# Kernel tuning notes

Hardware: AMD Instinct MI355X
Metric: run time of the kernel (lower is better)

Reference implementation:

```python
import jax, jax.numpy as jnp
import numpy as np

B, T, C, H = 4, 1024, 2048, 16
HD = C // H          # head dim = 128 (even, as RoPE requires)
BLOCK = 1024         # config.block_size == config.max_block_size
NEG = -1e30          # finite stand-in for -inf in the additive attention bias


def setup_inputs() -> dict:
    key = jax.random.key(0)
    k1, k2, k3, k4, k5 = jax.random.split(key, 5)
    x = jax.random.normal(k1, (B, T, C), jnp.float32)
    cumulative_scores = jax.random.uniform(k2, (B, T), jnp.float32)  # kept small: fed to exp()
    token_index = jax.random.randint(k3, (B, T), 0, BLOCK, dtype=jnp.int32)
    padding_mask = jnp.ones((B, T), jnp.int32)
    # xavier-ish scale so softmax doesn't saturate
    W_attn = jax.random.normal(k4, (C, 3 * C), jnp.float32) / np.sqrt(C)
    W_proj = jax.random.normal(k5, (C, C), jnp.float32) / np.sqrt(C)
    return dict(x=x, cumulative_scores=cumulative_scores, token_index=token_index,
                padding_mask=padding_mask, W_attn=W_attn, W_proj=W_proj)


def _rotate_half(a):
    a1, a2 = a[..., : HD // 2], a[..., HD // 2:]
    return jnp.concatenate([-a2, a1], axis=-1)


def reference(x, cumulative_scores, token_index, padding_mask, W_attn, W_proj):
    # QKV projection (bias=False per config)
    qkv = x @ W_attn                                  # (B,T,3C)
    q, k, v = jnp.split(qkv, 3, axis=2)
    heads = lambda a: a.reshape(B, T, H, HD).transpose(0, 2, 1, 3)  # (B,H,T,HD)
    q, k, v = heads(q), heads(k), heads(v)

    # input-dependent partial rotation positions (exact replica of the original
    # scatter: token_index (B,T) fancy-indexes the last axis of a (B,BLOCK)
    # buffer, so counts are summed over ALL batch rows, as in the source)
    counts = jnp.zeros((B, BLOCK), jnp.float32).at[..., token_index].add(1.0)
    t = jnp.cumsum(jnp.take_along_axis(1.0 / (counts + 1e-10), token_index, axis=-1), axis=-1)  # (B,T)

    # RoPE with per-token positions t (seq_dim=-2, offset 0 for both q and k)
    inv_freq = 1.0 / (10000.0 ** (jnp.arange(0, HD, 2, dtype=jnp.float32) / HD))
    freqs = jnp.einsum('bt,j->btj', t, inv_freq)
    emb = jnp.concatenate([freqs, freqs], axis=-1)[:, None, :, :]   # (B,1,T,HD)
    sin, cos = jnp.sin(emb), jnp.cos(emb)
    q = q * cos + _rotate_half(q) * sin
    k = k * cos + _rotate_half(k) * sin

    # 'fork' plan overrides on the last rotary channel
    q = q.at[..., -1].set(1.0)
    k = k.at[..., -1].set(jnp.broadcast_to(cumulative_scores[:, None, :], (B, H, T)))

    # V rescaled by exp(cumulative_scores)
    v = v * jnp.exp(cumulative_scores)[:, None, :, None]

    # causal + key-padding additive bias, SDPA with scale 1/sqrt(HD)
    keep = jnp.tril(jnp.ones((T, T), bool))[None, None] & padding_mask.astype(bool)[:, None, None, :]
    scores = jnp.einsum('bhqd,bhkd->bhqk', q, k) / np.sqrt(HD)
    scores = jnp.where(keep, scores, NEG)
    attn = jax.nn.softmax(scores, axis=-1)
    y = jnp.einsum('bhqk,bhkd->bhqd', attn, v)

    y = y.transpose(0, 2, 1, 3).reshape(B, T, C)
    return y @ W_proj
```

## Files before the change

kernel.cpp:

```cpp
#include <hip/hip_runtime.h>

#define BB 4
#define TT 1024
#define CCH 2048
#define HH 16
#define HDIM 128
#define NBLK 1024
#define MM (BB*TT)
#define N1 (3*CCH)
#define NQT 16

typedef _Float16 f16;
typedef _Float16 half8 __attribute__((ext_vector_type(8)));
typedef _Float16 half4 __attribute__((ext_vector_type(4)));
typedef float floatx4 __attribute__((ext_vector_type(4)));

__device__ __forceinline__ void g2lds16(const void* g, void* l) {
    __builtin_amdgcn_global_load_lds((const __attribute__((address_space(1))) void*)g,
                                     (__attribute__((address_space(3))) void*)l, 16, 0, 0);
}

__global__ void k_prep(const float* __restrict__ Wa, const float* __restrict__ Wp,
                       const float* __restrict__ x,
                       f16* __restrict__ WaT, f16* __restrict__ WpT,
                       f16* __restrict__ x16) {
    int z = blockIdx.z;
    if (z == 2) {
        int i = (blockIdx.y * 192 + blockIdx.x) * 256 + threadIdx.x + threadIdx.y * 32;
        if (i >= MM * CCH / 4) return;
        float4 v = ((const float4*)x)[i];
        union { ushort4 u; f16 h[4]; } o;
        o.h[0] = (f16)v.x; o.h[1] = (f16)v.y; o.h[2] = (f16)v.z; o.h[3] = (f16)v.w;
        ((ushort4*)x16)[i] = o.u;
        return;
    }
    const float* in = (z == 0) ? Wa : Wp;
    f16* out = (z == 0) ? WaT : WpT;
    int Cc = (z == 0) ? N1 : CCH;
    if (blockIdx.x * 32 >= Cc) return;
    __shared__ float tile[32][33];
    int c0 = blockIdx.x * 32, r0 = blockIdx.y * 32;
    int tx = threadIdx.x, ty = threadIdx.y;
#pragma unroll
    for (int k = 0; k < 4; k++) {
        int r = ty + k * 8;
        tile[r][tx] = in[(size_t)(r0 + r) * Cc + c0 + tx];
    }
    __syncthreads();
#pragma unroll
    for (int k = 0; k < 4; k++) {
        int r = ty + k * 8;
        out[(size_t)(c0 + r) * CCH + r0 + tx] = (f16)tile[tx][r];
    }
}

__global__ void k_trv(const f16* __restrict__ in, f16* __restrict__ out) {
    __shared__ f16 tile[32][34];
    int bh = blockIdx.z;
    int h0 = blockIdx.x * 32, t0 = blockIdx.y * 32;
    int tx = threadIdx.x, ty = threadIdx.y;
#pragma unroll
    for (int k = 0; k < 4; k++) {
        int t = ty + k * 8;
        tile[t][tx] = in[((size_t)bh * TT + t0 + t) * HDIM + h0 + tx];
    }
    __syncthreads();
#pragma unroll
    for (int k = 0; k < 4; k++) {
        int r = ty + k * 8;
        out[((size_t)bh * HDIM + h0 + r) * TT + t0 + tx] = tile[tx][r];
    }
}

__global__ void k_hist(const int* __restrict__ tok, int* __restrict__ cnt) {
    int i = blockIdx.x * blockDim.x + threadIdx.x;
    if (i < MM) atomicAdd(cnt + tok[i], 1);
}

__global__ __launch_bounds__(1024) void k_scan(const int* __restrict__ tok,
                                               const int* __restrict__ cnt,
                                               const int* __restrict__ pm,
                                               float* __restrict__ tpos,
                                               float* __restrict__ pb) {
    __shared__ float s[TT];
    int b = blockIdx.x, t = threadIdx.x;
    s[t] = 1.0f / ((float)cnt[tok[b * TT + t]] + 1e-10f);
    __syncthreads();
    for (int off = 1; off < TT; off <<= 1) {
        float add = (t >= off) ? s[t - off] : 0.0f;
        __syncthreads();
        s[t] += add;
        __syncthreads();
    }
    tpos[b * TT + t] = s[t];
    pb[b * TT + t] = pm[b * TT + t] ? 0.0f : -1e30f;
}

template <int MODE>
__global__ __launch_bounds__(256) void k_gemm(const f16* __restrict__ A,
                                              const f16* __restrict__ Bt,
                                              void* __restrict__ Cp,
                                              const float* __restrict__ tpos,
                                              const float* __restrict__ cs,
                                              f16* __restrict__ qr,
                                              f16* __restrict__ kr,
                                              f16* __restrict__ vsc,
                                              int Mdim, int Ndim, int Kdim) {
    const float SCALE = 0.08838834764831845f;
    __shared__ __align__(16) f16 As[128 * 32];
    __shared__ __align__(16) f16 Bs[128 * 32];
    int nbn = Ndim >> 7;
    int bm = blockIdx.x / nbn, bn = blockIdx.x % nbn;
    int tid = threadIdx.x;
    int w = tid >> 6, lane = tid & 63, quad = lane >> 4, l16 = lane & 15;
    int rsub = lane >> 2;
    int csub = (lane & 3) << 3;
    const f16* pa0 = A  + (size_t)((bm << 7) + w * 32 + rsub) * Kdim + csub;
    const f16* pa1 = pa0 + (size_t)16 * Kdim;
    const f16* pb0 = Bt + (size_t)((bn << 7) + w * 32 + rsub) * Kdim + csub;
    const f16* pb1 = pb0 + (size_t)16 * Kdim;
    floatx4 acc[2][8];
#pragma unroll
    for (int i = 0; i < 2; i++)
#pragma unroll
        for (int j = 0; j < 8; j++) acc[i][j] = (floatx4){0.f, 0.f, 0.f, 0.f};
    int nk = Kdim >> 5;
    for (int kt = 0; kt < nk; kt++) {
        __syncthreads();
        g2lds16(pa0, &As[(w * 32) * 32]);
        g2lds16(pa1, &As[(w * 32 + 16) * 32]);
        g2lds16(pb0, &Bs[(w * 32) * 32]);
        g2lds16(pb1, &Bs[(w * 32 + 16) * 32]);
        pa0 += 32; pa1 += 32; pb0 += 32; pb1 += 32;
        __syncthreads();
        half8 af[2], bfr[8];
#pragma unroll
        for (int i = 0; i < 2; i++) af[i] = *(const half8*)&As[(w * 32 + i * 16 + l16) * 32 + (quad << 3)];
#pragma unroll
        for (int j = 0; j < 8; j++) bfr[j] = *(const half8*)&Bs[(j * 16 + l16) * 32 + (quad << 3)];
#pragma unroll
        for (int i = 0; i < 2; i++)
#pragma unroll
            for (int j = 0; j < 8; j++)
                acc[i][j] = __builtin_amdgcn_mfma_f32_16x16x32_f16(af[i], bfr[j], acc[i][j], 0, 0, 0);
    }
    int row0 = (bm << 7) + w * 32 + (quad << 2);
    if (MODE == 0) {
        int cb = (bn << 7) + l16;
#pragma unroll
        for (int i = 0; i < 2; i++)
#pragma unroll
            for (int j = 0; j < 8; j++)
#pragma unroll
                for (int r = 0; r < 4; r++)
                    ((float*)Cp)[(size_t)(row0 + i * 16 + r) * Ndim + cb + j * 16] = acc[i][j][r];
    } else {
        int type = bn >> 4;
        int h = bn & 15;
        if (type < 2) {
            f16* outp = (type == 0) ? qr : kr;
            float invf[4];
#pragma unroll
            for (int jc = 0; jc < 4; jc++)
                invf[jc] = expf((float)(jc * 16 + l16) * -0.14391156929f);
#pragma unroll
            for (int i = 0; i < 2; i++)
#pragma unroll
                for (int r = 0; r < 4; r++) {
                    int row = row0 + i * 16 + r;
                    float tp = tpos[row], csv = cs[row];
                    size_t ob = ((size_t)((row >> 10) * HH + h) * TT + (row & 1023)) * HDIM + l16;
#pragma unroll
                    for (int jc = 0; jc < 4; jc++) {
                        float a1 = acc[i][jc][r], a2 = acc[i][jc + 4][r];
                        float sn, cn;
                        sincosf(tp * invf[jc], &sn, &cn);
                        float o1 = a1 * cn - a2 * sn, o2 = a2 * cn + a1 * sn;
                        if (type == 0) {
                            if (jc == 3 && l16 == 15) o2 = 1.0f;
                            o1 *= SCALE; o2 *= SCALE;
                        } else {
                            if (jc == 3 && l16 == 15) o2 = csv;
                        }
                        outp[ob + jc * 16]      = (f16)o1;
                        outp[ob + jc * 16 + 64] = (f16)o2;
                    }
                }
        } else {
#pragma unroll
            for (int i = 0; i < 2; i++)
#pragma unroll
                for (int r = 0; r < 4; r++) {
                    int row = row0 + i * 16 + r;
                    float ve = expf(cs[row]);
                    size_t ob = ((size_t)((row >> 10) * HH + h) * TT + (row & 1023)) * HDIM + l16;
#pragma unroll
                    for (int jc = 0; jc < 8; jc++)
                        vsc[ob + jc * 16] = (f16)(acc[i][jc][r] * ve);
                }
        }
    }
}

__global__ __launch_bounds__(256) void k_attn(const f16* __restrict__ qr,
                                              const f16* __restrict__ kr,
                                              const f16* __restrict__ vt,
                                              const float* __restrict__ pb,
                                              f16* __restrict__ y) {
    __shared__ __align__(16) f16 Ks[64 * 136];
    __shared__ __align__(16) f16 Vs[128 * 72];
    __shared__ float pbs[64];
    int p = blockIdx.x & (NQT / 2 - 1);
    int bh = blockIdx.x >> 3;
    int b = bh >> 4, h = bh & 15;
    int tid = threadIdx.x;
    int w = tid >> 6, lane = tid & 63, quad = lane >> 4, l16 = lane & 15;
#pragma unroll
    for (int pass = 0; pass < 2; pass++) {
        int qt = pass ? (NQT - 1 - p) : p;
        int q0 = qt << 6;
        int qg = q0 + w * 16 + l16;
        const f16* Qp = qr + ((size_t)bh * TT + qg) * HDIM;
        half8 qf[4];
#pragma unroll
        for (int kc = 0; kc < 4; kc++) qf[kc] = *(const half8*)&Qp[kc * 32 + (quad << 3)];
        floatx4 O[8];
#pragma unroll
        for (int i = 0; i < 8; i++) O[i] = (floatx4){0.f, 0.f, 0.f, 0.f};
        float mx = -1e30f, ls = 0.f;
        for (int kt = 0; kt <= qt; kt++) {
            __syncthreads();
            const f16* Kb = kr + ((size_t)bh * TT + (kt << 6)) * HDIM;
            const f16* Vb = vt + (size_t)bh * HDIM * TT + (kt << 6);
#pragma unroll
            for (int i = 0; i < 4; i++) {
                int seg = tid + (i << 8);
                int krow = seg >> 4, kcol = (seg & 15) << 3;
                *(uint4*)&Ks[krow * 136 + kcol] = *(const uint4*)&Kb[(size_t)krow * HDIM + kcol];
                int vrow = seg >> 3, vcol = (seg & 7) << 3;
                *(uint4*)&Vs[vrow * 72 + vcol] = *(const uint4*)&Vb[(size_t)vrow * TT + vcol];
            }
            if (tid < 64) pbs[tid] = pb[b * TT + (kt << 6) + tid];
            __syncthreads();
            floatx4 Sv[4];
#pragma unroll
            for (int mc = 0; mc < 4; mc++) Sv[mc] = (floatx4){0.f, 0.f, 0.f, 0.f};
#pragma unroll
            for (int kc = 0; kc < 4; kc++)
#pragma unroll
                for (int mc = 0; mc < 4; mc++) {
                    half8 kf = *(const half8*)&Ks[(mc * 16 + l16) * 136 + kc * 32 + (quad << 3)];
                    Sv[mc] = __builtin_amdgcn_mfma_f32_16x16x32_f16(kf, qf[kc], Sv[mc], 0, 0, 0);
                }
            float pv[4][4];
            float mnew = mx;
#pragma unroll
            for (int mc = 0; mc < 4; mc++) {
                float4 pbv = *(const float4*)&pbs[mc * 16 + (quad << 2)];
#pragma unroll
                for (int i = 0; i < 4; i++) {
                    int kv = (kt << 6) + mc * 16 + (quad << 2) + i;
                    float s = (kv <= qg) ? Sv[mc][i] + ((const float*)&pbv)[i] : -1e30f;
                    pv[mc][i] = s;
                    mnew = fmaxf(mnew, s);
                }
            }
            mnew = fmaxf(mnew, __shfl_xor(mnew, 16));
            mnew = fmaxf(mnew, __shfl_xor(mnew, 32));
            float al = __expf(mx - mnew);
            mx = mnew;
            float psum = 0.f;
#pragma unroll
            for (int mc = 0; mc < 4; mc++)
#pragma unroll
                for (int i = 0; i < 4; i++) {
                    float e = __expf(pv[mc][i] - mnew);
                    pv[mc][i] = e;
                    psum += e;
                }
            psum += __shfl_xor(psum, 16);
            psum += __shfl_xor(psum, 32);
            ls = ls * al + psum;
#pragma unroll
            for (int hm = 0; hm < 8; hm++)
#pragma unroll
                for (int i = 0; i < 4; i++) O[hm][i] *= al;
            half4 pf[4];
#pragma unroll
            for (int mc = 0; mc < 4; mc++) {
                pf[mc][0] = (f16)pv[mc][0]; pf[mc][1] = (f16)pv[mc][1];
                pf[mc][2] = (f16)pv[mc][2]; pf[mc][3] = (f16)pv[mc][3];
            }
#pragma unroll
            for (int mc = 0; mc < 4; mc++)
#pragma unroll
                for (int hm = 0; hm < 8; hm++) {
                    half4 vf = *(const half4*)&Vs[(hm * 16 + l16) * 72 + mc * 16 + (quad << 2)];
                    O[hm] = __builtin_amdgcn_mfma_f32_16x16x16f16(vf, pf[mc], O[hm], 0, 0, 0);
                }
        }
        float inv = 1.0f / ls;
#pragma unroll
        for (int hm = 0; hm < 8; hm++) {
            half4 ov;
#pragma unroll
            for (int i = 0; i < 4; i++) ov[i] = (f16)(O[hm][i] * inv);
            *(half4*)&y[((size_t)b * TT + qg) * CCH + h * HDIM + hm * 16 + (quad << 2)] = ov;
        }
        __syncthreads();
    }
}

extern "C" void kernel_launch(void* const* d_in, const int* in_sizes, int n_in,
                              void* d_out, int out_size, void* d_ws, size_t ws_size,
                              hipStream_t stream) {
    const float* x   = (const float*)d_in[0];
    const float* cs  = (const float*)d_in[1];
    const int*   tok = (const int*)d_in[2];
    const int*   pm  = (const int*)d_in[3];
    const float* Wa  = (const float*)d_in[4];
    const float* Wp  = (const float*)d_in[5];
    float* out = (float*)d_out;
    char* ws = (char*)d_ws;

    f16* x16 = (f16*)(ws + 0);
    f16* WaT = (f16*)(ws + 16777216);
    f16* vt  = (f16*)(ws + 41943040);
    f16* WpT = (f16*)(ws + 58720256);
    f16* qr  = (f16*)(ws + 92274688);
    f16* kr  = (f16*)(ws + 109051904);
    f16* vsc = (f16*)(ws + 125829120);
    int*   cnt  = (int*)(ws + 142606336);
    float* tpos = (float*)(ws + 142610432);
    float* pb   = (float*)(ws + 142626816);
    f16* y   = x16;

    hipMemsetAsync(cnt, 0, NBLK * sizeof(int), stream);
    k_hist<<<MM / 256, 256, 0, stream>>>(tok, cnt);
    k_scan<<<BB, TT, 0, stream>>>(tok, cnt, pm, tpos, pb);
    k_prep<<<dim3(N1 / 32, CCH / 32, 3), dim3(32, 8), 0, stream>>>(Wa, Wp, x, WaT, WpT, x16);
    k_gemm<1><<<(MM / 128) * (N1 / 128), 256, 0, stream>>>(x16, WaT, nullptr, tpos, cs,
                                                           qr, kr, vsc, MM, N1, CCH);
    k_trv<<<dim3(4, 32, BB * HH), dim3(32, 8), 0, stream>>>(vsc, vt);
    k_attn<<<BB * HH * (NQT / 2), 256, 0, stream>>>(qr, kr, vt, pb, y);
    k_gemm<0><<<(MM / 128) * (CCH / 128), 256, 0, stream>>>(y, WpT, out, nullptr, nullptr,
                                                            nullptr, nullptr, nullptr, MM, CCH, CCH);
}
```

Measured before the change: 420.3 us.

## Replace GEMM with 256x256 double-buffered, swizzled, 8-wave pipelined kernel and RoPE table

Rewrites both projection GEMMs as a 256x256-tile, 512-thread kernel. It double-buffers LDS through global_load_lds, interleaves staging of the next K tiles with MFMA quarters, and uses an XOR swizzle to avoid LDS bank conflicts. A chiplet-aware block remap groups blocks by XCD. RoPE sin/cos is precomputed into a table by a new small kernel instead of calling sincosf in the GEMM epilogue. The aim is higher MFMA utilisation and less global load latency, at the cost of much more LDS per block (128KB), fewer blocks (384 and 128 on a 256-CU part), and fragile hand-written wait counts.

```diff
diff --git a/kernel.cpp b/kernel.cpp
--- a/kernel.cpp
+++ b/kernel.cpp
@@ -96,107 +96,197 @@
     pb[b * TT + t] = pm[b * TT + t] ? 0.0f : -1e30f;
 }
 
+__global__ void k_rope(const float* __restrict__ tpos, float2* __restrict__ tab) {
+    int i = blockIdx.x * 256 + threadIdx.x;
+    int row = i >> 6, j = i & 63;
+    float f = tpos[row] * expf((float)j * -0.14391156929f);
+    float sn, cn; sincosf(f, &sn, &cn);
+    tab[i] = make_float2(cn, sn);
+}
+
+#define RA(buf, mf, kk) (*(const half8*)((const char*)As + ((buf) << 15) + ((aoffb + ((mf) << 11) + ((kk) << 6)) ^ flip)))
+#define RB(buf, nf, kk) (*(const half8*)((const char*)Bs + ((buf) << 15) + ((boffb + ((nf) << 13) + ((kk) << 6)) ^ flip)))
+#define STAGE(P, L, h, t) do { \
+    g2lds16((P) + (size_t)(((h) << 7) + ro0) * 2048 + ((t) << 6) + co0, (L) + ((h) << 13) + (w << 9)); \
+    g2lds16((P) + (size_t)(((h) << 7) + ro1) * 2048 + ((t) << 6) + co1, (L) + ((h) << 13) + ((8 + w) << 9)); \
+} while (0)
+#define MFMAQ(AF, BF, M0, N0) do { \
+  _Pragma("unroll") for (int m_ = 0; m_ < 4; m_++) \
+  _Pragma("unroll") for (int n_ = 0; n_ < 2; n_++) \
+  _Pragma("unroll") for (int k_ = 0; k_ < 2; k_++) \
+    acc[(M0) + m_][(N0) + n_] = __builtin_amdgcn_mfma_f32_16x16x32_f16(AF[m_][k_], BF[n_][k_], acc[(M0) + m_][(N0) + n_], 0, 0, 0); \
+} while (0)
+#define BAR() __builtin_amdgcn_s_barrier()
+#define WLG0() asm volatile("s_waitcnt lgkmcnt(0)" ::: "memory")
+
 template <int MODE>
-__global__ __launch_bounds__(256) void k_gemm(const f16* __restrict__ A,
-                                              const f16* __restrict__ Bt,
-                                              void* __restrict__ Cp,
-                                              const float* __restrict__ tpos,
-                                              const float* __restrict__ cs,
-                                              f16* __restrict__ qr,
-                                              f16* __restrict__ kr,
-                                              f16* __restrict__ vsc,
-                                              int Mdim, int Ndim, int Kdim) {
+__global__ __launch_bounds__(512, 2) void k_gemm8(const f16* __restrict__ A,
+                                                  const f16* __restrict__ Bt,
+                                                  float* __restrict__ Cp,
+                                                  const float2* __restrict__ tab,
+                                                  const float* __restrict__ cs,
+                                                  f16* __restrict__ qr,
+                                                  f16* __restrict__ kr,
+                                                  f16* __restrict__ vsc) {
     const float SCALE = 0.08838834764831845f;
-    __shared__ __align__(16) f16 As[128 * 32];
-    __shared__ __align__(16) f16 Bs[128 * 32];
-    int nbn = Ndim >> 7;
-    int bm = blockIdx.x / nbn, bn = blockIdx.x % nbn;
+    const int NBN = MODE ? 24 : 8;
+    const int NWG = MODE ? 384 : 128;
+    const int CPX = NWG >> 3;
+    __shared__ __align__(16) f16 As[2 * 16384];
+    __shared__ __align__(16) f16 Bs[2 * 16384];
+
+    int bid = blockIdx.x;
+    int s = (bid & 7) * CPX + (bid >> 3);
+    int bm = s / NBN, bn = s % NBN;
+
     int tid = threadIdx.x;
     int w = tid >> 6, lane = tid & 63, quad = lane >> 4, l16 = lane & 15;
-    int rsub = lane >> 2;
-    int csub = (lane & 3) << 3;
-    const f16* pa0 = A  + (size_t)((bm << 7) + w * 32 + rsub) * Kdim + csub;
-    const f16* pa1 = pa0 + (size_t)16 * Kdim;
-    const f16* pb0 = Bt + (size_t)((bn << 7) + w * 32 + rsub) * Kdim + csub;
-    const f16* pb1 = pb0 + (size_t)16 * Kdim;
-    floatx4 acc[2][8];
-#pragma unroll
-    for (int i = 0; i < 2; i++)
-#pragma unroll
-        for (int j = 0; j < 8; j++) acc[i][j] = (floatx4){0.f, 0.f, 0.f, 0.f};
-    int nk = Kdim >> 5;
-    for (int kt = 0; kt < nk; kt++) {
-        __syncthreads();
-        g2lds16(pa0, &As[(w * 32) * 32]);
-        g2lds16(pa1, &As[(w * 32 + 16) * 32]);
-        g2lds16(pb0, &Bs[(w * 32) * 32]);
-        g2lds16(pb1, &Bs[(w * 32 + 16) * 32]);
-        pa0 += 32; pa1 += 32; pb0 += 32; pb1 += 32;
-        __syncthreads();
-        half8 af[2], bfr[8];
-#pragma unroll
-        for (int i = 0; i < 2; i++) af[i] = *(const half8*)&As[(w * 32 + i * 16 + l16) * 32 + (quad << 3)];
-#pragma unroll
-        for (int j = 0; j < 8; j++) bfr[j] = *(const half8*)&Bs[(j * 16 + l16) * 32 + (quad << 3)];
-#pragma unroll
-        for (int i = 0; i < 2; i++)
-#pragma unroll
-            for (int j = 0; j < 8; j++)
-                acc[i][j] = __builtin_amdgcn_mfma_f32_16x16x32_f16(af[i], bfr[j], acc[i][j], 0, 0, 0);
-    }
-    int row0 = (bm << 7) + w * 32 + (quad << 2);
+    int wm = w >> 2, wn = w & 3;
+
+    const f16* Ab = A + (size_t)(bm << 8) * 2048;
+    const f16* Bb = Bt + (size_t)(bn << 8) * 2048;
+
+    int db0 = (w << 10) + (lane << 4);
+    int db1 = ((8 + w) << 10) + (lane << 4);
+    int sb0 = db0 ^ (((db0 >> 9) & 1) << 5);
+    int sb1 = db1 ^ (((db1 >> 9) & 1) << 5);
+    int ro0 = sb0 >> 7, co0 = (sb0 & 127) >> 1;
+    int ro1 = sb1 >> 7, co1 = (sb1 & 127) >> 1;
+
+    const int flip = (l16 & 4) << 3;
+    const int aoffb = ((wm * 128 + l16) << 7) + (quad << 4);
+    const int boffb = ((wn * 16 + l16) << 7) + (quad << 4);
+
+    floatx4 acc[8][4];
+#pragma unroll
+    for (int i = 0; i < 8; i++)
+#pragma unroll
+        for (int j = 0; j < 4; j++) acc[i][j] = (floatx4){0.f, 0.f, 0.f, 0.f};
+
+    STAGE(Bb, Bs, 0, 0);
+    STAGE(Ab, As, 0, 0);
+    STAGE(Ab, As, 1, 0);
+    STAGE(Bb, Bs, 1, 0);
+    STAGE(Bb, Bs + 16384, 0, 1);
+    STAGE(Ab, As + 16384, 0, 1);
+    STAGE(Ab, As + 16384, 1, 1);
+    asm volatile("s_waitcnt vmcnt(6)" ::: "memory");
+    BAR();
+
+#pragma unroll 1
+    for (int it = 0; it < 16; ++it) {
+        const int t1 = 2 * it + 1, t2 = 2 * it + 2, t3 = 2 * it + 3;
+        const bool g2 = (t2 < 32), g3 = (t3 < 32);
+        half8 af0[4][2], af1[4][2], bf0[2][2], bf1[2][2];
+#pragma unroll
+        for (int m = 0; m < 4; m++) { af0[m][0] = RA(0, m, 0); af0[m][1] = RA(0, m, 1); }
+#pragma unroll
+        for (int n = 0; n < 2; n++) { bf0[n][0] = RB(0, n, 0); bf0[n][1] = RB(0, n, 1); }
+        STAGE(Bb, Bs + 16384, 1, t1);
+        asm volatile("s_waitcnt lgkmcnt(8)" ::: "memory");
+        BAR(); WLG0();
+        __builtin_amdgcn_s_setprio(1); MFMAQ(af0, bf0, 0, 0); __builtin_amdgcn_s_setprio(0);
+        BAR();
+#pragma unroll
+        for (int m = 0; m < 4; m++) { af1[m][0] = RA(0, 4 + m, 0); af1[m][1] = RA(0, 4 + m, 1); }
+        if (g2) STAGE(Bb, Bs, 0, t2);
+        BAR(); WLG0();
+        __builtin_amdgcn_s_setprio(1); MFMAQ(af1, bf0, 4, 0); __builtin_amdgcn_s_setprio(0);
+        BAR();
+#pragma unroll
+        for (int n = 0; n < 2; n++) { bf1[n][0] = RB(0, 2 + n, 0); bf1[n][1] = RB(0, 2 + n, 1); }
+        if (g2) STAGE(Ab, As, 0, t2);
+        BAR(); WLG0();
+        __builtin_amdgcn_s_setprio(1); MFMAQ(af1, bf1, 4, 2); __builtin_amdgcn_s_setprio(0);
+        BAR();
+        if (g2) STAGE(Ab, As, 1, t2);
+        BAR();
+        __builtin_amdgcn_s_setprio(1); MFMAQ(af0, bf1, 0, 2); __builtin_amdgcn_s_setprio(0);
+        if (it < 15) { asm volatile("s_waitcnt vmcnt(6)" ::: "memory"); }
+        else         { asm volatile("s_waitcnt vmcnt(0)" ::: "memory"); }
+        BAR();
+#pragma unroll
+        for (int m = 0; m < 4; m++) { af0[m][0] = RA(1, m, 0); af0[m][1] = RA(1, m, 1); }
+#pragma unroll
+        for (int n = 0; n < 2; n++) { bf0[n][0] = RB(1, n, 0); bf0[n][1] = RB(1, n, 1); }
+        if (g2) STAGE(Bb, Bs, 1, t2);
+        asm volatile("s_waitcnt lgkmcnt(8)" ::: "memory");
+        BAR(); WLG0();
+        __builtin_amdgcn_s_setprio(1); MFMAQ(af0, bf0, 0, 0); __builtin_amdgcn_s_setprio(0);
+        BAR();
+#pragma unroll
+        for (int m = 0; m < 4; m++) { af1[m][0] = RA(1, 4 + m, 0); af1[m][1] = RA(1, 4 + m, 1); }
+        if (g3) STAGE(Bb, Bs + 16384, 0, t3);
+        BAR(); WLG0();
+        __builtin_amdgcn_s_setprio(1); MFMAQ(af1, bf0, 4, 0); __builtin_amdgcn_s_setprio(0);
+        BAR();
+#pragma unroll
+        for (int n = 0; n < 2; n++) { bf1[n][0] = RB(1, 2 + n, 0); bf1[n][1] = RB(1, 2 + n, 1); }
+        if (g3) STAGE(Ab, As + 16384, 0, t3);
+        BAR(); WLG0();
+        __builtin_amdgcn_s_setprio(1); MFMAQ(af1, bf1, 4, 2); __builtin_amdgcn_s_setprio(0);
+        BAR();
+        if (g3) STAGE(Ab, As + 16384, 1, t3);
+        BAR();
+        __builtin_amdgcn_s_setprio(1); MFMAQ(af0, bf1, 0, 2); __builtin_amdgcn_s_setprio(0);
+        if (it < 15) { asm volatile("s_waitcnt vmcnt(6)" ::: "memory"); }
+        else         { asm volatile("s_waitcnt vmcnt(0)" ::: "memory"); }
+        BAR();
+    }
+
     if (MODE == 0) {
-        int cb = (bn << 7) + l16;
-#pragma unroll
-        for (int i = 0; i < 2; i++)
-#pragma unroll
-            for (int j = 0; j < 8; j++)
-#pragma unroll
-                for (int r = 0; r < 4; r++)
-                    ((float*)Cp)[(size_t)(row0 + i * 16 + r) * Ndim + cb + j * 16] = acc[i][j][r];
+#pragma unroll
+        for (int mf = 0; mf < 8; mf++)
+#pragma unroll
+            for (int nf = 0; nf < 4; nf++) {
+                int col = (bn << 8) + wn * 16 + nf * 64 + l16;
+#pragma unroll
+                for (int r = 0; r < 4; r++) {
+                    int row = (bm << 8) + wm * 128 + mf * 16 + (quad << 2) + r;
+                    Cp[(size_t)row * CCH + col] = acc[mf][nf][r];
+                }
+            }
     } else {
-        int type = bn >> 4;
-        int h = bn & 15;
+        int type = bn >> 3;
+        int h0 = (bn * 2) & 15;
+        int d1 = wn * 16 + l16;
         if (type < 2) {
             f16* outp = (type == 0) ? qr : kr;
-            float invf[4];
-#pragma unroll
-            for (int jc = 0; jc < 4; jc++)
-                invf[jc] = expf((float)(jc * 16 + l16) * -0.14391156929f);
-#pragma unroll
-            for (int i = 0; i < 2; i++)
+#pragma unroll
+            for (int mf = 0; mf < 8; mf++)
 #pragma unroll
                 for (int r = 0; r < 4; r++) {
-                    int row = row0 + i * 16 + r;
-                    float tp = tpos[row], csv = cs[row];
-                    size_t ob = ((size_t)((row >> 10) * HH + h) * TT + (row & 1023)) * HDIM + l16;
-#pragma unroll
-                    for (int jc = 0; jc < 4; jc++) {
-                        float a1 = acc[i][jc][r], a2 = acc[i][jc + 4][r];
-                        float sn, cn;
-                        sincosf(tp * invf[jc], &sn, &cn);
-                        float o1 = a1 * cn - a2 * sn, o2 = a2 * cn + a1 * sn;
+                    int row = (bm << 8) + wm * 128 + mf * 16 + (quad << 2) + r;
+                    float2 tc = tab[row * 64 + d1];
+#pragma unroll
+                    for (int p = 0; p < 2; p++) {
+                        float a1 = acc[mf][2 * p][r], a2 = acc[mf][2 * p + 1][r];
+                        float o1 = a1 * tc.x - a2 * tc.y;
+                        float o2 = a2 * tc.x + a1 * tc.y;
                         if (type == 0) {
-                            if (jc == 3 && l16 == 15) o2 = 1.0f;
+                            if (d1 == 63) o2 = 1.0f;
                             o1 *= SCALE; o2 *= SCALE;
                         } else {
-                            if (jc == 3 && l16 == 15) o2 = csv;
+                            if (d1 == 63) o2 = cs[row];
                         }
-                        outp[ob + jc * 16]      = (f16)o1;
-                        outp[ob + jc * 16 + 64] = (f16)o2;
+                        size_t ob = ((size_t)((row >> 10) * HH + h0 + p) * TT + (row & 1023)) * HDIM + d1;
+                        outp[ob] = (f16)o1;
+                        outp[ob + 64] = (f16)o2;
                     }
                 }
         } else {
 #pragma unroll
-            for (int i = 0; i < 2; i++)
+            for (int mf = 0; mf < 8; mf++)
 #pragma unroll
                 for (int r = 0; r < 4; r++) {
-                    int row = row0 + i * 16 + r;
-                    float ve = expf(cs[row]);
-                    size_t ob = ((size_t)((row >> 10) * HH + h) * TT + (row & 1023)) * HDIM + l16;
-#pragma unroll
-                    for (int jc = 0; jc < 8; jc++)
-                        vsc[ob + jc * 16] = (f16)(acc[i][jc][r] * ve);
+                    int row = (bm << 8) + wm * 128 + mf * 16 + (quad << 2) + r;
+                    float ve = __expf(cs[row]);
+#pragma unroll
+                    for (int nf = 0; nf < 4; nf++) {
+                        int d = ((nf & 1) << 6) + d1;
+                        size_t ob = ((size_t)((row >> 10) * HH + h0 + (nf >> 1)) * TT + (row & 1023)) * HDIM + d;
+                        vsc[ob] = (f16)(acc[mf][nf][r] * ve);
+                    }
                 }
         }
     }
@@ -327,6 +417,7 @@
     f16* WaT = (f16*)(ws + 16777216);
     f16* vt  = (f16*)(ws + 41943040);
     f16* WpT = (f16*)(ws + 58720256);
+    float2* tab = (float2*)(ws + 67108864);
     f16* qr  = (f16*)(ws + 92274688);
     f16* kr  = (f16*)(ws + 109051904);
     f16* vsc = (f16*)(ws + 125829120);
@@ -338,11 +429,10 @@
     hipMemsetAsync(cnt, 0, NBLK * sizeof(int), stream);
     k_hist<<<MM / 256, 256, 0, stream>>>(tok, cnt);
     k_scan<<<BB, TT, 0, stream>>>(tok, cnt, pm, tpos, pb);
+    k_rope<<<MM * 64 / 256, 256, 0, stream>>>(tpos, tab);
     k_prep<<<dim3(N1 / 32, CCH / 32, 3), dim3(32, 8), 0, stream>>>(Wa, Wp, x, WaT, WpT, x16);
-    k_gemm<1><<<(MM / 128) * (N1 / 128), 256, 0, stream>>>(x16, WaT, nullptr, tpos, cs,
-                                                           qr, kr, vsc, MM, N1, CCH);
+    k_gemm8<1><<<384, 512, 0, stream>>>(x16, WaT, nullptr, tab, cs, qr, kr, vsc);
     k_trv<<<dim3(4, 32, BB * HH), dim3(32, 8), 0, stream>>>(vsc, vt);
     k_attn<<<BB * HH * (NQT / 2), 256, 0, stream>>>(qr, kr, vt, pb, y);
-    k_gemm<0><<<(MM / 128) * (CCH / 128), 256, 0, stream>>>(y, WpT, out, nullptr, nullptr,
-                                                            nullptr, nullptr, nullptr, MM, CCH, CCH);
-}
+    k_gemm8<0><<<128, 512, 0, stream>>>(y, WpT, out, nullptr, nullptr, nullptr, nullptr, nullptr);
+}
```

Result: slower. 454.3 us (+8.1%).
